# Optimization experiments

Measured on AMD Instinct MI355X. Metric: run time of the kernel, lower is better.

## Reference

```python
import jax, jax.numpy as jnp
import numpy as np

HIDDEN = 16  # hk.LSTM(16)


def lstm_scan(x, W, b, reverse):
    """Haiku LSTM unroll. x: [B,T,D]; W: [D+H, 4H]; b: [4H]. Returns [B,T,H]."""
    B = x.shape[0]

    def step(carry, xt):
        h, c = carry
        gated = jnp.concatenate([xt, h], axis=-1) @ W + b
        i, g, f, o = jnp.split(gated, 4, axis=-1)
        f = jax.nn.sigmoid(f + 1.0)  # haiku forget-gate bias of +1
        c = f * c + jax.nn.sigmoid(i) * jnp.tanh(g)
        h = jax.nn.sigmoid(o) * jnp.tanh(c)
        return (h, c), h

    init = (jnp.zeros((B, HIDDEN), x.dtype), jnp.zeros((B, HIDDEN), x.dtype))
    xt = jnp.swapaxes(x, 0, 1)  # [T,B,D] time-major for scan
    _, outs = jax.lax.scan(step, init, xt, reverse=reverse)
    return jnp.swapaxes(outs, 0, 1)  # [B,T,H]


def setup_inputs() -> dict:
    key = jax.random.key(0)
    ks = jax.random.split(key, 8)
    B, T, D = 4096, 256, 20
    E, H, M, OUT = 64, HIDDEN, 16, 2

    def glorot(k, shape):
        fan_in = shape[0]
        return (jax.random.normal(k, shape, jnp.float32) / np.sqrt(fan_in)).astype(jnp.float32)

    return {
        "x": jax.random.normal(ks[0], (B, T, D), jnp.float32),
        "W0": glorot(ks[1], (D, E)), "b0": jnp.zeros((E,), jnp.float32),
        "Wf": glorot(ks[2], (E + H, 4 * H)), "bf": jnp.zeros((4 * H,), jnp.float32),
        "Wb": glorot(ks[3], (E + H, 4 * H)), "bb": jnp.zeros((4 * H,), jnp.float32),
        "W1": glorot(ks[4], (2 * H, E)), "b1": jnp.zeros((E,), jnp.float32),
        "W2": glorot(ks[5], (E, M)), "b2": jnp.zeros((M,), jnp.float32),
        "W3": glorot(ks[6], (M, OUT)), "b3": jnp.zeros((OUT,), jnp.float32),
    }


def reference(x, W0, b0, Wf, bf, Wb, bb, W1, b1, W2, b2, W3, b3):
    h = jax.nn.relu(x @ W0 + b0)                 # [B,T,64]
    fwd = lstm_scan(h, Wf, bf, reverse=False)    # [B,T,16]
    bwd = lstm_scan(h, Wb, bb, reverse=True)     # [B,T,16], output[t] uses future state
    outs = jnp.concatenate([fwd, bwd], axis=-1)[:, -1, :]  # take last time step, [B,32]
    outs = jax.nn.relu(outs @ W1 + b1)
    outs = jax.nn.relu(outs @ W2 + b2)
    return outs @ W3 + b3
```

## Files before the change

kernel.cpp:

```cpp
#include <hip/hip_runtime.h>


typedef __attribute__((ext_vector_type(8))) short short8;
typedef __attribute__((ext_vector_type(4))) float floatx4;

union F8 { uint32_t u[4]; short8 v; };

#define LDW 66

__device__ __forceinline__ float tanh_fast(float x) {
    float e = __expf(-2.f * x);
    return __fdividef(2.f, 1.f + e) - 1.f;
}

#define ROT(v, S) __int_as_float(__builtin_amdgcn_mov_dpp(__float_as_int(v), 0x120 | (S), 0xf, 0xf, false))

__device__ __forceinline__ void split_pack(const float* f, uint32_t* hi, uint32_t* lo) {
#pragma unroll
    for (int i = 0; i < 4; ++i) {
        uint32_t u0 = __float_as_uint(f[2 * i]), u1 = __float_as_uint(f[2 * i + 1]);
        hi[i] = (u0 >> 16) | (u1 & 0xFFFF0000u);
        float r0 = f[2 * i]     - __uint_as_float(u0 & 0xFFFF0000u);
        float r1 = f[2 * i + 1] - __uint_as_float(u1 & 0xFFFF0000u);
        uint32_t v0 = __float_as_uint(r0), v1 = __float_as_uint(r1);
        lo[i] = (v0 >> 16) | (v1 & 0xFFFF0000u);
    }
}

__global__ __launch_bounds__(64, 2)
void bilstm_fused(const float* __restrict__ x,
                  const float* __restrict__ W0, const float* __restrict__ b0,
                  const float* __restrict__ Wf, const float* __restrict__ bf,
                  const float* __restrict__ Wb, const float* __restrict__ bb,
                  const float* __restrict__ W1, const float* __restrict__ b1,
                  const float* __restrict__ W2, const float* __restrict__ b2,
                  const float* __restrict__ W3, const float* __restrict__ b3,
                  float* __restrict__ out)
{
    __shared__ __align__(16) float lds_xh[16 * LDW];
    __shared__ __align__(16) float lds_g [16 * LDW];
    __shared__ __align__(16) float h_sh[48];

    const int j    = threadIdx.x;
    const int b    = blockIdx.x;
    const int nl   = j & 15;
    const int quad = j >> 4;

    int rot1 = __builtin_amdgcn_mov_dpp(j, 0x121, 0xf, 0xf, false);
    const bool plus = ((rot1 & 15) == ((nl + 1) & 15));

    float wfhp[16];
#pragma unroll
    for (int s = 0; s < 16; ++s) {
        const int srcq = plus ? ((nl + s) & 15) : ((nl + 16 - s) & 15);
        wfhp[s] = Wf[(64 + srcq) * 64 + j];
    }

    F8 B1h[4], B1l[4];
#pragma unroll
    for (int T = 0; T < 4; ++T) {
        float w[8];
#pragma unroll
        for (int e = 0; e < 8; ++e) {
            int k = quad * 8 + e;
            w[e] = (k < 20) ? W0[k * 64 + T * 16 + nl] : 0.f;
        }
        split_pack(w, B1h[T].u, B1l[T].u);
    }
    F8 B2h[4][2], B2l[4][2];
#pragma unroll
    for (int T = 0; T < 4; ++T)
#pragma unroll
        for (int KH = 0; KH < 2; ++KH) {
            float w[8];
#pragma unroll
            for (int e = 0; e < 8; ++e) {
                int k = KH * 32 + quad * 8 + e;
                w[e] = Wf[k * 64 + T * 16 + nl];
            }
            split_pack(w, B2h[T][KH].u, B2l[T][KH].u);
        }

    float b0v[4], bfv[4];
#pragma unroll
    for (int T = 0; T < 4; ++T) {
        b0v[T] = b0[T * 16 + nl];
        bfv[T] = bf[T * 16 + nl];
    }

    const float gmul  = (quad == 1) ? -2.f : -1.f;
    const float gbias = (quad == 2) ? 1.f : 0.f;
    const float amul  = (quad == 1) ? 2.f : 1.f;
    const float aadd  = (quad == 1) ? -1.f : 0.f;
    const bool  b0sel = (quad & 1) != 0;
    const bool  b1sel = (quad & 2) != 0;

    float c = 0.f, hh = 0.f;
    const float* xb = x + (size_t)b * (256 * 20);

#pragma unroll 1
    for (int ch = 0; ch < 16; ++ch) {
        const int t0 = ch * 16;

        const float* xrow = xb + (size_t)(t0 + nl) * 20;
        float xk[8];
#pragma unroll
        for (int e = 0; e < 8; ++e) {
            int k = quad * 8 + e;
            xk[e] = (k < 20) ? xrow[k] : 0.f;
        }
        F8 A1h, A1l;
        split_pack(xk, A1h.u, A1l.u);

        floatx4 acc1[4];
#pragma unroll
        for (int T = 0; T < 4; ++T) acc1[T] = (floatx4){b0v[T], b0v[T], b0v[T], b0v[T]};
#pragma unroll
        for (int T = 0; T < 4; ++T) {
            acc1[T] = __builtin_amdgcn_mfma_f32_16x16x32_bf16(A1h.v, B1h[T].v, acc1[T], 0, 0, 0);
            acc1[T] = __builtin_amdgcn_mfma_f32_16x16x32_bf16(A1l.v, B1h[T].v, acc1[T], 0, 0, 0);
            acc1[T] = __builtin_amdgcn_mfma_f32_16x16x32_bf16(A1h.v, B1l[T].v, acc1[T], 0, 0, 0);
        }

#pragma unroll
        for (int T = 0; T < 4; ++T)
#pragma unroll
            for (int reg = 0; reg < 4; ++reg)
                lds_xh[(quad * 4 + reg) * LDW + T * 16 + nl] = fmaxf(acc1[T][reg], 0.f);
        __builtin_amdgcn_wave_barrier();

        F8 A2h[2], A2l[2];
#pragma unroll
        for (int KH = 0; KH < 2; ++KH) {
            float xe[8];
#pragma unroll
            for (int e = 0; e < 8; ++e)
                xe[e] = lds_xh[nl * LDW + KH * 32 + quad * 8 + e];
            split_pack(xe, A2h[KH].u, A2l[KH].u);
        }

        floatx4 acc2[4];
#pragma unroll
        for (int T = 0; T < 4; ++T) acc2[T] = (floatx4){bfv[T], bfv[T], bfv[T], bfv[T]};
#pragma unroll
        for (int T = 0; T < 4; ++T)
#pragma unroll
            for (int KH = 0; KH < 2; ++KH) {
                acc2[T] = __builtin_amdgcn_mfma_f32_16x16x32_bf16(A2h[KH].v, B2h[T][KH].v, acc2[T], 0, 0, 0);
                acc2[T] = __builtin_amdgcn_mfma_f32_16x16x32_bf16(A2l[KH].v, B2h[T][KH].v, acc2[T], 0, 0, 0);
                acc2[T] = __builtin_amdgcn_mfma_f32_16x16x32_bf16(A2h[KH].v, B2l[T][KH].v, acc2[T], 0, 0, 0);
            }

#pragma unroll
        for (int T = 0; T < 4; ++T)
#pragma unroll
            for (int reg = 0; reg < 4; ++reg)
                lds_g[(quad * 4 + reg) * LDW + T * 16 + nl] = acc2[T][reg];
        __builtin_amdgcn_wave_barrier();

        float gcur = lds_g[j];
#pragma unroll
        for (int tau = 0; tau < 16; ++tau) {
            float gnext = lds_g[((tau < 15) ? (tau + 1) : 15) * LDW + j];

            float v0 = hh * wfhp[0];
            float v1 = ROT(hh, 1) * wfhp[1];
            float v2 = ROT(hh, 2) * wfhp[2];
            float v3 = ROT(hh, 3) * wfhp[3];
            v0 = fmaf(ROT(hh, 4),  wfhp[4],  v0);
            v1 = fmaf(ROT(hh, 5),  wfhp[5],  v1);
            v2 = fmaf(ROT(hh, 6),  wfhp[6],  v2);
            v3 = fmaf(ROT(hh, 7),  wfhp[7],  v3);
            v0 = fmaf(ROT(hh, 8),  wfhp[8],  v0);
            v1 = fmaf(ROT(hh, 9),  wfhp[9],  v1);
            v2 = fmaf(ROT(hh, 10), wfhp[10], v2);
            v3 = fmaf(ROT(hh, 11), wfhp[11], v3);
            v0 = fmaf(ROT(hh, 12), wfhp[12], v0);
            v1 = fmaf(ROT(hh, 13), wfhp[13], v1);
            v2 = fmaf(ROT(hh, 14), wfhp[14], v2);
            v3 = fmaf(ROT(hh, 15), wfhp[15], v3);
            float gated = gcur + ((v0 + v1) + (v2 + v3));

            float e = __expf(gmul * (gated + gbias));
            float y = __fdividef(1.f, 1.f + e);
            float a = fmaf(y, amul, aadd);

            float d1 = __shfl_xor(a, 16);
            float d2 = __shfl_xor(a, 32);
            float d3 = __shfl_xor(a, 48);
            float lo  = b0sel ? d1 : a;
            float hi  = b0sel ? d3 : d2;
            float lo1 = b0sel ? a  : d1;
            float hi1 = b0sel ? d2 : d3;
            float ai = b1sel ? hi  : lo;
            float ag = b1sel ? hi1 : lo1;
            float af = b1sel ? lo  : hi;
            float ao = b1sel ? lo1 : hi1;

            c  = fmaf(af, c, ai * ag);
            hh = ao * tanh_fast(c);
            gcur = gnext;
        }
    }

    if (j < 16) h_sh[j] = hh;
    __builtin_amdgcn_wave_barrier();

    {
        float u0 = bb[j], u1 = 0.f, u2 = 0.f, u3 = 0.f;
        const float* xr = &lds_xh[15 * LDW];
#pragma unroll
        for (int k4 = 0; k4 < 16; ++k4) {
            float q0 = xr[4 * k4 + 0], q1 = xr[4 * k4 + 1];
            float q2 = xr[4 * k4 + 2], q3 = xr[4 * k4 + 3];
            u0 = fmaf(q0, Wb[(4 * k4 + 0) * 64 + j], u0);
            u1 = fmaf(q1, Wb[(4 * k4 + 1) * 64 + j], u1);
            u2 = fmaf(q2, Wb[(4 * k4 + 2) * 64 + j], u2);
            u3 = fmaf(q3, Wb[(4 * k4 + 3) * 64 + j], u3);
        }
        float gated = (u0 + u1) + (u2 + u3);
        float e = __expf(gmul * gated);
        float y = __fdividef(1.f, 1.f + e);
        float a = fmaf(y, amul, aadd);
        float ai = __shfl(a, nl, 64);
        float ag = __shfl(a, nl + 16, 64);
        float ao = __shfl(a, nl + 48, 64);
        float cb = ai * ag;
        float hb = ao * tanh_fast(cb);
        __builtin_amdgcn_wave_barrier();
        if (j < 16) h_sh[16 + j] = hb;
        __builtin_amdgcn_wave_barrier();
    }

    {
        float u0 = b1[j], u1 = 0.f, u2 = 0.f, u3 = 0.f;
        const float4* hs = (const float4*)h_sh;
#pragma unroll
        for (int k4 = 0; k4 < 8; ++k4) {
            float4 v = hs[k4];
            u0 = fmaf(v.x, W1[(4 * k4 + 0) * 64 + j], u0);
            u1 = fmaf(v.y, W1[(4 * k4 + 1) * 64 + j], u1);
            u2 = fmaf(v.z, W1[(4 * k4 + 2) * 64 + j], u2);
            u3 = fmaf(v.w, W1[(4 * k4 + 3) * 64 + j], u3);
        }
        float l1 = fmaxf((u0 + u1) + (u2 + u3), 0.f);
        __builtin_amdgcn_wave_barrier();
        lds_g[j] = l1;
        __builtin_amdgcn_wave_barrier();

        if (j < 16) {
            float v0 = b2[j], v1 = 0.f, v2 = 0.f, v3 = 0.f;
            const float4* ls = (const float4*)lds_g;
#pragma unroll
            for (int k4 = 0; k4 < 16; ++k4) {
                float4 v = ls[k4];
                v0 = fmaf(v.x, W2[(4 * k4 + 0) * 16 + j], v0);
                v1 = fmaf(v.y, W2[(4 * k4 + 1) * 16 + j], v1);
                v2 = fmaf(v.z, W2[(4 * k4 + 2) * 16 + j], v2);
                v3 = fmaf(v.w, W2[(4 * k4 + 3) * 16 + j], v3);
            }
            h_sh[32 + j] = fmaxf((v0 + v1) + (v2 + v3), 0.f);
        }
        __builtin_amdgcn_wave_barrier();

        if (j < 2) {
            float o = b3[j];
#pragma unroll
            for (int k = 0; k < 16; ++k)
                o = fmaf(h_sh[32 + k], W3[k * 2 + j], o);
            out[b * 2 + j] = o;
        }
    }
}

extern "C" void kernel_launch(void* const* d_in, const int* in_sizes, int n_in,
                              void* d_out, int out_size, void* d_ws, size_t ws_size,
                              hipStream_t stream) {
    const float* x  = (const float*)d_in[0];
    const float* W0 = (const float*)d_in[1];
    const float* b0 = (const float*)d_in[2];
    const float* Wf = (const float*)d_in[3];
    const float* bf = (const float*)d_in[4];
    const float* Wb = (const float*)d_in[5];
    const float* bb = (const float*)d_in[6];
    const float* W1 = (const float*)d_in[7];
    const float* b1 = (const float*)d_in[8];
    const float* W2 = (const float*)d_in[9];
    const float* b2 = (const float*)d_in[10];
    const float* W3 = (const float*)d_in[11];
    const float* b3 = (const float*)d_in[12];
    float* outp = (float*)d_out;

    hipLaunchKernelGGL(bilstm_fused, dim3(4096), dim3(64), 0, stream,
                       x, W0, b0, Wf, bf, Wb, bb, W1, b1, W2, b2, W3, b3, outp);
}
```

Baseline: 312.3 us.

## Split input projection into separate GEMM kernel and stream gates into scan

The fused per-sequence kernel is split in two. A parallel GEMM kernel first computes the input-to-gate pre-activations (relu projection plus the LSTM input matmul, with the forget-gate +1 folded into the bias) for all timesteps into a 256 MB workspace. A scan kernel with 4 waves per block then runs only the recurrence, prefetching gate rows from global memory 8 steps ahead. This takes the MFMA work off the serial critical path and raises occupancy, at the cost of a large HBM write and read round trip. The old fused kernel remains as a fallback when the workspace is too small.

```diff
diff --git a/kernel.cpp b/kernel.cpp
--- a/kernel.cpp
+++ b/kernel.cpp
@@ -27,15 +27,292 @@
     }
 }
 
+__global__ __launch_bounds__(256, 2)
+void gpre_gemm(const float* __restrict__ x,
+               const float* __restrict__ W0, const float* __restrict__ b0,
+               const float* __restrict__ Wf, const float* __restrict__ bf,
+               float* __restrict__ gpre)
+{
+    __shared__ __align__(16) float xtile[64 * 20];
+    __shared__ __align__(16) float xh_t[4][16 * LDW];
+
+    const int tid  = threadIdx.x;
+    const int wv   = tid >> 6;
+    const int j    = tid & 63;
+    const int nl   = j & 15;
+    const int quad = j >> 4;
+    const int r0   = blockIdx.x * 64;
+
+    {
+        const float4* src = (const float4*)(x + (size_t)r0 * 20);
+        float4* dst = (float4*)xtile;
+        if (tid < 256)       dst[tid]       = src[tid];
+        if (tid < 64)        dst[tid + 256] = src[tid + 256];
+    }
+    __syncthreads();
+
+    F8 B1h[4], B1l[4];
+#pragma unroll
+    for (int T = 0; T < 4; ++T) {
+        float w[8];
+#pragma unroll
+        for (int e = 0; e < 8; ++e) {
+            int k = quad * 8 + e;
+            w[e] = (k < 20) ? W0[k * 64 + T * 16 + nl] : 0.f;
+        }
+        split_pack(w, B1h[T].u, B1l[T].u);
+    }
+    F8 B2h[4][2], B2l[4][2];
+#pragma unroll
+    for (int T = 0; T < 4; ++T)
+#pragma unroll
+        for (int KH = 0; KH < 2; ++KH) {
+            float w[8];
+#pragma unroll
+            for (int e = 0; e < 8; ++e) {
+                int k = KH * 32 + quad * 8 + e;
+                w[e] = Wf[k * 64 + T * 16 + nl];
+            }
+            split_pack(w, B2h[T][KH].u, B2l[T][KH].u);
+        }
+
+    float xk[8];
+#pragma unroll
+    for (int e = 0; e < 8; ++e) {
+        int k = quad * 8 + e;
+        xk[e] = (k < 20) ? xtile[(wv * 16 + nl) * 20 + k] : 0.f;
+    }
+    F8 A1h, A1l;
+    split_pack(xk, A1h.u, A1l.u);
+
+    floatx4 acc1[4];
+#pragma unroll
+    for (int T = 0; T < 4; ++T) {
+        float bv = b0[T * 16 + nl];
+        acc1[T] = (floatx4){bv, bv, bv, bv};
+    }
+#pragma unroll
+    for (int T = 0; T < 4; ++T) {
+        acc1[T] = __builtin_amdgcn_mfma_f32_16x16x32_bf16(A1h.v, B1h[T].v, acc1[T], 0, 0, 0);
+        acc1[T] = __builtin_amdgcn_mfma_f32_16x16x32_bf16(A1l.v, B1h[T].v, acc1[T], 0, 0, 0);
+        acc1[T] = __builtin_amdgcn_mfma_f32_16x16x32_bf16(A1h.v, B1l[T].v, acc1[T], 0, 0, 0);
+    }
+
+#pragma unroll
+    for (int T = 0; T < 4; ++T)
+#pragma unroll
+        for (int reg = 0; reg < 4; ++reg)
+            xh_t[wv][(quad * 4 + reg) * LDW + T * 16 + nl] = fmaxf(acc1[T][reg], 0.f);
+    __builtin_amdgcn_wave_barrier();
+
+    F8 A2h[2], A2l[2];
+#pragma unroll
+    for (int KH = 0; KH < 2; ++KH) {
+        float xe[8];
+#pragma unroll
+        for (int e = 0; e < 8; ++e)
+            xe[e] = xh_t[wv][nl * LDW + KH * 32 + quad * 8 + e];
+        split_pack(xe, A2h[KH].u, A2l[KH].u);
+    }
+
+    floatx4 acc2[4];
+#pragma unroll
+    for (int T = 0; T < 4; ++T) {
+        float bv = bf[T * 16 + nl] + ((T == 2) ? 1.f : 0.f);
+        acc2[T] = (floatx4){bv, bv, bv, bv};
+    }
+#pragma unroll
+    for (int T = 0; T < 4; ++T)
+#pragma unroll
+        for (int KH = 0; KH < 2; ++KH) {
+            acc2[T] = __builtin_amdgcn_mfma_f32_16x16x32_bf16(A2h[KH].v, B2h[T][KH].v, acc2[T], 0, 0, 0);
+            acc2[T] = __builtin_amdgcn_mfma_f32_16x16x32_bf16(A2l[KH].v, B2h[T][KH].v, acc2[T], 0, 0, 0);
+            acc2[T] = __builtin_amdgcn_mfma_f32_16x16x32_bf16(A2h[KH].v, B2l[T][KH].v, acc2[T], 0, 0, 0);
+        }
+
+    float* gp = gpre + (size_t)(r0 + wv * 16) * 64;
+#pragma unroll
+    for (int T = 0; T < 4; ++T)
+#pragma unroll
+        for (int reg = 0; reg < 4; ++reg)
+            gp[(quad * 4 + reg) * 64 + T * 16 + nl] = acc2[T][reg];
+}
+
+__global__ __launch_bounds__(256, 4)
+void lstm_scan(const float* __restrict__ gpre,
+               const float* __restrict__ x,
+               const float* __restrict__ W0, const float* __restrict__ b0,
+               const float* __restrict__ Wf,
+               const float* __restrict__ Wb, const float* __restrict__ bb,
+               const float* __restrict__ W1, const float* __restrict__ b1,
+               const float* __restrict__ W2, const float* __restrict__ b2,
+               const float* __restrict__ W3, const float* __restrict__ b3,
+               float* __restrict__ out)
+{
+    __shared__ __align__(16) float xh_sh[4][64];
+    __shared__ __align__(16) float h_sh[4][48];
+
+    const int wv   = threadIdx.x >> 6;
+    const int j    = threadIdx.x & 63;
+    const int b    = blockIdx.x * 4 + wv;
+    const int nl   = j & 15;
+    const int quad = j >> 4;
+
+    int rot1 = __builtin_amdgcn_mov_dpp(j, 0x121, 0xf, 0xf, false);
+    const bool plus = ((rot1 & 15) == ((nl + 1) & 15));
+
+    float wfhp[16];
+#pragma unroll
+    for (int s = 0; s < 16; ++s) {
+        const int srcq = plus ? ((nl + s) & 15) : ((nl + 16 - s) & 15);
+        wfhp[s] = Wf[(64 + srcq) * 64 + j];
+    }
+
+    const float gmul  = (quad == 1) ? -2.f : -1.f;
+    const float amul  = (quad == 1) ? 2.f : 1.f;
+    const float aadd  = (quad == 1) ? -1.f : 0.f;
+    const bool  b0sel = (quad & 1) != 0;
+    const bool  b1sel = (quad & 2) != 0;
+
+    float c = 0.f, hh = 0.f;
+    const float* gb = gpre + (size_t)b * (256 * 64);
+
+    float gbuf[8];
+#pragma unroll
+    for (int i = 0; i < 8; ++i) gbuf[i] = gb[i * 64 + j];
+
+#pragma unroll 1
+    for (int t = 0; t < 256; t += 8) {
+#pragma unroll
+        for (int i = 0; i < 8; ++i) {
+            float gated0 = gbuf[i];
+            {
+                int tf = t + 8 + i; tf = (tf > 255) ? 255 : tf;
+                gbuf[i] = gb[tf * 64 + j];
+            }
+            float v0 = hh * wfhp[0];
+            float v1 = ROT(hh, 1) * wfhp[1];
+            float v2 = ROT(hh, 2) * wfhp[2];
+            float v3 = ROT(hh, 3) * wfhp[3];
+            v0 = fmaf(ROT(hh, 4),  wfhp[4],  v0);
+            v1 = fmaf(ROT(hh, 5),  wfhp[5],  v1);
+            v2 = fmaf(ROT(hh, 6),  wfhp[6],  v2);
+            v3 = fmaf(ROT(hh, 7),  wfhp[7],  v3);
+            v0 = fmaf(ROT(hh, 8),  wfhp[8],  v0);
+            v1 = fmaf(ROT(hh, 9),  wfhp[9],  v1);
+            v2 = fmaf(ROT(hh, 10), wfhp[10], v2);
+            v3 = fmaf(ROT(hh, 11), wfhp[11], v3);
+            v0 = fmaf(ROT(hh, 12), wfhp[12], v0);
+            v1 = fmaf(ROT(hh, 13), wfhp[13], v1);
+            v2 = fmaf(ROT(hh, 14), wfhp[14], v2);
+            v3 = fmaf(ROT(hh, 15), wfhp[15], v3);
+            float gated = gated0 + ((v0 + v1) + (v2 + v3));
+
+            float e = __expf(gmul * gated);
+            float y = __fdividef(1.f, 1.f + e);
+            float a = fmaf(y, amul, aadd);
+
+            float d1 = __shfl_xor(a, 16);
+            float d2 = __shfl_xor(a, 32);
+            float d3 = __shfl_xor(a, 48);
+            float lo  = b0sel ? d1 : a;
+            float hi  = b0sel ? d3 : d2;
+            float lo1 = b0sel ? a  : d1;
+            float hi1 = b0sel ? d2 : d3;
+            float ai = b1sel ? hi  : lo;
+            float ag = b1sel ? hi1 : lo1;
+            float af = b1sel ? lo  : hi;
+            float ao = b1sel ? lo1 : hi1;
+
+            c  = fmaf(af, c, ai * ag);
+            hh = ao * tanh_fast(c);
+        }
+    }
+
+    {
+        const float* xr = x + (size_t)b * (256 * 20) + 255 * 20;
+        float s = b0[j];
+#pragma unroll
+        for (int k = 0; k < 20; ++k) s = fmaf(xr[k], W0[k * 64 + j], s);
+        xh_sh[wv][j] = fmaxf(s, 0.f);
+        if (j < 16) h_sh[wv][j] = hh;
+    }
+    __builtin_amdgcn_wave_barrier();
+
+    {
+        float u0 = bb[j], u1 = 0.f, u2 = 0.f, u3 = 0.f;
+        const float* xr = xh_sh[wv];
+#pragma unroll
+        for (int k4 = 0; k4 < 16; ++k4) {
+            u0 = fmaf(xr[4 * k4 + 0], Wb[(4 * k4 + 0) * 64 + j], u0);
+            u1 = fmaf(xr[4 * k4 + 1], Wb[(4 * k4 + 1) * 64 + j], u1);
+            u2 = fmaf(xr[4 * k4 + 2], Wb[(4 * k4 + 2) * 64 + j], u2);
+            u3 = fmaf(xr[4 * k4 + 3], Wb[(4 * k4 + 3) * 64 + j], u3);
+        }
+        float gated = (u0 + u1) + (u2 + u3);
+        float e = __expf(gmul * gated);
+        float y = __fdividef(1.f, 1.f + e);
+        float a = fmaf(y, amul, aadd);
+        float ai = __shfl(a, nl, 64);
+        float ag = __shfl(a, nl + 16, 64);
+        float ao = __shfl(a, nl + 48, 64);
+        float cb = ai * ag;
+        float hb = ao * tanh_fast(cb);
+        __builtin_amdgcn_wave_barrier();
+        if (j < 16) h_sh[wv][16 + j] = hb;
+        __builtin_amdgcn_wave_barrier();
+    }
+
+    {
+        float u0 = b1[j], u1 = 0.f, u2 = 0.f, u3 = 0.f;
+        const float4* hs = (const float4*)h_sh[wv];
+#pragma unroll
+        for (int k4 = 0; k4 < 8; ++k4) {
+            float4 v = hs[k4];
+            u0 = fmaf(v.x, W1[(4 * k4 + 0) * 64 + j], u0);
+            u1 = fmaf(v.y, W1[(4 * k4 + 1) * 64 + j], u1);
+            u2 = fmaf(v.z, W1[(4 * k4 + 2) * 64 + j], u2);
+            u3 = fmaf(v.w, W1[(4 * k4 + 3) * 64 + j], u3);
+        }
+        float l1 = fmaxf((u0 + u1) + (u2 + u3), 0.f);
+        __builtin_amdgcn_wave_barrier();
+        xh_sh[wv][j] = l1;
+        __builtin_amdgcn_wave_barrier();
+
+        if (j < 16) {
+            float v0 = b2[j], v1 = 0.f, v2 = 0.f, v3 = 0.f;
+            const float4* ls = (const float4*)xh_sh[wv];
+#pragma unroll
+            for (int k4 = 0; k4 < 16; ++k4) {
+                float4 v = ls[k4];
+                v0 = fmaf(v.x, W2[(4 * k4 + 0) * 16 + j], v0);
+                v1 = fmaf(v.y, W2[(4 * k4 + 1) * 16 + j], v1);
+                v2 = fmaf(v.z, W2[(4 * k4 + 2) * 16 + j], v2);
+                v3 = fmaf(v.w, W2[(4 * k4 + 3) * 16 + j], v3);
+            }
+            h_sh[wv][32 + j] = fmaxf((v0 + v1) + (v2 + v3), 0.f);
+        }
+        __builtin_amdgcn_wave_barrier();
+
+        if (j < 2) {
+            float o = b3[j];
+#pragma unroll
+            for (int k = 0; k < 16; ++k)
+                o = fmaf(h_sh[wv][32 + k], W3[k * 2 + j], o);
+            out[b * 2 + j] = o;
+        }
+    }
+}
+
 __global__ __launch_bounds__(64, 2)
-void bilstm_fused(const float* __restrict__ x,
-                  const float* __restrict__ W0, const float* __restrict__ b0,
-                  const float* __restrict__ Wf, const float* __restrict__ bf,
-                  const float* __restrict__ Wb, const float* __restrict__ bb,
-                  const float* __restrict__ W1, const float* __restrict__ b1,
-                  const float* __restrict__ W2, const float* __restrict__ b2,
-                  const float* __restrict__ W3, const float* __restrict__ b3,
-                  float* __restrict__ out)
+void bilstm_fused_r4(const float* __restrict__ x,
+                     const float* __restrict__ W0, const float* __restrict__ b0,
+                     const float* __restrict__ Wf, const float* __restrict__ bf,
+                     const float* __restrict__ Wb, const float* __restrict__ bb,
+                     const float* __restrict__ W1, const float* __restrict__ b1,
+                     const float* __restrict__ W2, const float* __restrict__ b2,
+                     const float* __restrict__ W3, const float* __restrict__ b3,
+                     float* __restrict__ out)
 {
     __shared__ __align__(16) float lds_xh[16 * LDW];
     __shared__ __align__(16) float lds_g [16 * LDW];
@@ -101,7 +378,6 @@
 #pragma unroll 1
     for (int ch = 0; ch < 16; ++ch) {
         const int t0 = ch * 16;
-
         const float* xrow = xb + (size_t)(t0 + nl) * 20;
         float xk[8];
 #pragma unroll
@@ -121,7 +397,6 @@
             acc1[T] = __builtin_amdgcn_mfma_f32_16x16x32_bf16(A1l.v, B1h[T].v, acc1[T], 0, 0, 0);
             acc1[T] = __builtin_amdgcn_mfma_f32_16x16x32_bf16(A1h.v, B1l[T].v, acc1[T], 0, 0, 0);
         }
-
 #pragma unroll
         for (int T = 0; T < 4; ++T)
 #pragma unroll
@@ -150,7 +425,6 @@
                 acc2[T] = __builtin_amdgcn_mfma_f32_16x16x32_bf16(A2l[KH].v, B2h[T][KH].v, acc2[T], 0, 0, 0);
                 acc2[T] = __builtin_amdgcn_mfma_f32_16x16x32_bf16(A2h[KH].v, B2l[T][KH].v, acc2[T], 0, 0, 0);
             }
-
 #pragma unroll
         for (int T = 0; T < 4; ++T)
 #pragma unroll
@@ -162,7 +436,6 @@
 #pragma unroll
         for (int tau = 0; tau < 16; ++tau) {
             float gnext = lds_g[((tau < 15) ? (tau + 1) : 15) * LDW + j];
-
             float v0 = hh * wfhp[0];
             float v1 = ROT(hh, 1) * wfhp[1];
             float v2 = ROT(hh, 2) * wfhp[2];
@@ -211,12 +484,10 @@
         const float* xr = &lds_xh[15 * LDW];
 #pragma unroll
         for (int k4 = 0; k4 < 16; ++k4) {
-            float q0 = xr[4 * k4 + 0], q1 = xr[4 * k4 + 1];
-            float q2 = xr[4 * k4 + 2], q3 = xr[4 * k4 + 3];
-            u0 = fmaf(q0, Wb[(4 * k4 + 0) * 64 + j], u0);
-            u1 = fmaf(q1, Wb[(4 * k4 + 1) * 64 + j], u1);
-            u2 = fmaf(q2, Wb[(4 * k4 + 2) * 64 + j], u2);
-            u3 = fmaf(q3, Wb[(4 * k4 + 3) * 64 + j], u3);
+            u0 = fmaf(xr[4 * k4 + 0], Wb[(4 * k4 + 0) * 64 + j], u0);
+            u1 = fmaf(xr[4 * k4 + 1], Wb[(4 * k4 + 1) * 64 + j], u1);
+            u2 = fmaf(xr[4 * k4 + 2], Wb[(4 * k4 + 2) * 64 + j], u2);
+            u3 = fmaf(xr[4 * k4 + 3], Wb[(4 * k4 + 3) * 64 + j], u3);
         }
         float gated = (u0 + u1) + (u2 + u3);
         float e = __expf(gmul * gated);
@@ -291,6 +562,15 @@
     const float* b3 = (const float*)d_in[12];
     float* outp = (float*)d_out;
 
-    hipLaunchKernelGGL(bilstm_fused, dim3(4096), dim3(64), 0, stream,
-                       x, W0, b0, Wf, bf, Wb, bb, W1, b1, W2, b2, W3, b3, outp);
+    const size_t need = (size_t)4096 * 256 * 64 * sizeof(float);
+    if (ws_size >= need) {
+        float* gpre = (float*)d_ws;
+        hipLaunchKernelGGL(gpre_gemm, dim3(16384), dim3(256), 0, stream,
+                           x, W0, b0, Wf, bf, gpre);
+        hipLaunchKernelGGL(lstm_scan, dim3(1024), dim3(256), 0, stream,
+                           gpre, x, W0, b0, Wf, Wb, bb, W1, b1, W2, b2, W3, b3, outp);
+    } else {
+        hipLaunchKernelGGL(bilstm_fused_r4, dim3(4096), dim3(64), 0, stream,
+                           x, W0, b0, Wf, bf, Wb, bb, W1, b1, W2, b2, W3, b3, outp);
+    }
 }
```

New measurement: 406.7 us. +30.2%, slower.
